# Performance work log

Measured on AMD Instinct MI355X. Metric: run time of the kernel, lower is better.

## Reference

```python
import jax, jax.numpy as jnp
import numpy as np

B, N, D = 4, 512, 128
TAU = 0.5
EPS = 1e-9

def setup_inputs() -> dict:
    key = jax.random.key(0)
    ks = jax.random.split(key, 6)
    sc = 0.05  # weight scale for numerical sanity
    return {
        "entity_states": jax.random.normal(ks[0], (B, N, D), dtype=jnp.float32),
        "Wp": jax.random.normal(ks[1], (D, D), dtype=jnp.float32) * sc,
        "bp": jnp.zeros((D,), dtype=jnp.float32),
        "edge_logits": jax.random.normal(ks[2], (N, N), dtype=jnp.float32),
        "W1": jax.random.normal(ks[3], (2 * D, D), dtype=jnp.float32) * sc,
        "b1": jnp.zeros((D,), dtype=jnp.float32),
        "W2": jax.random.normal(ks[4], (D, D), dtype=jnp.float32) * sc,
        "b2": jnp.zeros((D,), dtype=jnp.float32),
        "u_noise": jax.random.uniform(ks[5], (N, N), dtype=jnp.float32),
    }

def reference(entity_states, Wp, bp, edge_logits, W1, b1, W2, b2, u_noise):
    b, n, d = entity_states.shape
    # entity projection
    proj = entity_states @ Wp + bp  # (B,N,D)
    # gumbel-softmax adjacency (row-wise softmax over sources)
    g = -jnp.log(-jnp.log(u_noise + EPS) + EPS)
    A = jax.nn.softmax((edge_logits + g) / TAU, axis=-1)  # (N,N)
    # split concat-MLP first layer: combined = [source_j, target_i]
    W1_src, W1_tgt = W1[:d], W1[d:]
    s = proj @ W1_src  # (B,N,D) contribution of source j
    t = proj @ W1_tgt  # (B,N,D) contribution of target i
    # h[b,i,j,:] = relu(s[b,j] + t[b,i] + b1)
    h = jax.nn.relu(s[:, None, :, :] + t[:, :, None, :] + b1)  # (B,N,N,D)
    msg = h @ W2 + b2  # (B,N,N,D)
    # weighted aggregation over sources j with A[i,j]
    upd = jnp.einsum('ij,bijd->bid', A, msg)  # (B,N,D)
    next_state = entity_states + upd
    return next_state, jnp.broadcast_to(A, (b, n, n))
```

## Files before the change

kernel.cpp:

```cpp
#include <hip/hip_runtime.h>
#include <math.h>

#define Bv 4
#define Nv 512
#define Dv 128
#define BND (Bv*Nv*Dv)
#define NN  (Nv*Nv)
#define EPSv 1e-9f

typedef float f4 __attribute__((ext_vector_type(4)));

__device__ __forceinline__ f4 relu4(f4 z) {
#if __has_builtin(__builtin_elementwise_max)
    return __builtin_elementwise_max(z, (f4)0.0f);
#else
    z.x = fmaxf(z.x, 0.0f); z.y = fmaxf(z.y, 0.0f);
    z.z = fmaxf(z.z, 0.0f); z.w = fmaxf(z.w, 0.0f);
    return z;
#endif
}

__global__ __launch_bounds__(256) void k_prep(
    const float* __restrict__ ES, const float* __restrict__ Wp,
    const float* __restrict__ bp, const float* __restrict__ W1,
    const float* __restrict__ b1, const float* __restrict__ EL,
    const float* __restrict__ UN,
    float* __restrict__ s_out, float* __restrict__ t_out,
    float* __restrict__ A_out)
{
    __shared__ float es[4][Dv];
    __shared__ float pr[4][Dv];
    __shared__ float sred[4];
    const int bi = blockIdx.x;
    const int t  = threadIdx.x;

    {
        const int row = bi;
        const float u0 = UN[row*Nv + t];
        const float u1 = UN[row*Nv + t + 256];
        const float g0 = -logf(-logf(u0 + EPSv) + EPSv);
        const float g1 = -logf(-logf(u1 + EPSv) + EPSv);
        const float z0 = (EL[row*Nv + t]       + g0) * 2.0f;
        const float z1 = (EL[row*Nv + t + 256] + g1) * 2.0f;

        float m = fmaxf(z0, z1);
        #pragma unroll
        for (int off = 32; off >= 1; off >>= 1)
            m = fmaxf(m, __shfl_xor(m, off, 64));
        if ((t & 63) == 0) sred[t >> 6] = m;
        __syncthreads();
        m = fmaxf(fmaxf(sred[0], sred[1]), fmaxf(sred[2], sred[3]));

        const float e0 = expf(z0 - m);
        const float e1 = expf(z1 - m);
        float ssum = e0 + e1;
        #pragma unroll
        for (int off = 32; off >= 1; off >>= 1)
            ssum += __shfl_xor(ssum, off, 64);
        __syncthreads();
        if ((t & 63) == 0) sred[t >> 6] = ssum;
        __syncthreads();
        const float inv = 1.0f / (sred[0] + sred[1] + sred[2] + sred[3]);
        const float a0 = e0 * inv;
        const float a1 = e1 * inv;
        #pragma unroll
        for (int bb = 0; bb < Bv; ++bb) {
            A_out[bb*NN + row*Nv + t]       = a0;
            A_out[bb*NN + row*Nv + t + 256] = a1;
        }
    }

    const int row0 = bi * 4;
    const int c  = t & 127;
    const int rg = t >> 7;

    for (int idx = t; idx < 4*Dv; idx += 256)
        es[idx >> 7][idx & 127] = ES[(row0 + (idx >> 7))*Dv + (idx & 127)];
    __syncthreads();

    {
        float acc[2];
        const float bpc = bp[c];
        acc[0] = bpc; acc[1] = bpc;
        #pragma unroll 8
        for (int k = 0; k < Dv; ++k) {
            const float w = Wp[k*Dv + c];
            acc[0] = fmaf(es[rg*2][k],   w, acc[0]);
            acc[1] = fmaf(es[rg*2+1][k], w, acc[1]);
        }
        pr[rg*2][c]   = acc[0];
        pr[rg*2+1][c] = acc[1];
    }
    __syncthreads();

    float sacc0 = b1[c], sacc1 = sacc0, tacc0 = 0.0f, tacc1 = 0.0f;
    #pragma unroll 8
    for (int k = 0; k < Dv; ++k) {
        const float ws_ = W1[k*Dv + c];
        const float wt_ = W1[(Dv + k)*Dv + c];
        const float p0 = pr[rg*2][k];
        const float p1 = pr[rg*2+1][k];
        sacc0 = fmaf(p0, ws_, sacc0);
        sacc1 = fmaf(p1, ws_, sacc1);
        tacc0 = fmaf(p0, wt_, tacc0);
        tacc1 = fmaf(p1, wt_, tacc1);
    }
    const int ra = (row0 + rg*2)*Dv + c;
    s_out[ra]      = sacc0;
    s_out[ra + Dv] = sacc1;
    t_out[ra]      = tacc0;
    t_out[ra + Dv] = tacc1;
}

__global__ __launch_bounds__(256) void k_main(
    const float* __restrict__ s_buf, const float* __restrict__ t_buf,
    const float* __restrict__ A0,    const float* __restrict__ ES,
    const float* __restrict__ W2,    const float* __restrict__ b2,
    float* __restrict__ out)
{
    __shared__ float A_lds[8][Nv];
    __shared__ f4    part[8][8][32];
    __shared__ float hsum[8][Dv];
    const int i0 = blockIdx.x * 8;
    const int b  = blockIdx.y;
    const int t  = threadIdx.x;
    const int dq = t & 31;
    const int jg = t >> 5;

    {
        const f4* __restrict__ src = (const f4*)(A0 + i0*Nv);
        f4* dst = (f4*)(&A_lds[0][0]);
        #pragma unroll
        for (int u = 0; u < 4; ++u)
            dst[t + u*256] = src[t + u*256];
    }

    f4 tv[8];
    #pragma unroll
    for (int r = 0; r < 8; ++r)
        tv[r] = *(const f4*)(t_buf + (b*Nv + i0 + r)*Dv + dq*4);

    f4 acc[8];
    #pragma unroll
    for (int r = 0; r < 8; ++r) acc[r] = (f4)0.0f;

    __syncthreads();

    const float* __restrict__ sb = s_buf + (size_t)b*Nv*Dv + dq*4;
    const int j0 = jg*64;
    for (int j4 = j0; j4 < j0 + 64; j4 += 4) {
        f4 a[8];
        #pragma unroll
        for (int r = 0; r < 8; ++r)
            a[r] = *(const f4*)(&A_lds[r][j4]);
        #pragma unroll
        for (int u = 0; u < 4; ++u) {
            const f4 sv = *(const f4*)(sb + (j4 + u)*Dv);
            #pragma unroll
            for (int r = 0; r < 8; ++r) {
                f4 z = relu4(sv + tv[r]);
                acc[r] += a[r][u] * z;
            }
        }
    }

    #pragma unroll
    for (int r = 0; r < 8; ++r) part[jg][r][dq] = acc[r];
    __syncthreads();
    {
        const int ri = t >> 5;
        f4 s = part[0][ri][dq];
        #pragma unroll
        for (int g = 1; g < 8; ++g) s += part[g][ri][dq];
        *(f4*)(&hsum[ri][dq*4]) = s;
    }
    __syncthreads();

    const int cg = t & 63;
    const int rg = t >> 6;
    const int c0 = 2*cg;
    const int r0 = 2*rg;
    float o00 = b2[c0], o01 = b2[c0+1];
    float o10 = o00,    o11 = o01;
    for (int k4 = 0; k4 < Dv; k4 += 4) {
        const f4 h0 = *(const f4*)(&hsum[r0][k4]);
        const f4 h1 = *(const f4*)(&hsum[r0+1][k4]);
        #pragma unroll
        for (int u = 0; u < 4; ++u) {
            const float2 w = *(const float2*)(W2 + (k4 + u)*Dv + c0);
            o00 = fmaf(h0[u], w.x, o00);
            o01 = fmaf(h0[u], w.y, o01);
            o10 = fmaf(h1[u], w.x, o10);
            o11 = fmaf(h1[u], w.y, o11);
        }
    }
    const int ro0 = (b*Nv + i0 + r0)*Dv + c0;
    const int ro1 = ro0 + Dv;
    const float2 e0 = *(const float2*)(ES + ro0);
    const float2 e1 = *(const float2*)(ES + ro1);
    float2 v0, v1;
    v0.x = e0.x + o00; v0.y = e0.y + o01;
    v1.x = e1.x + o10; v1.y = e1.y + o11;
    *(float2*)(out + ro0) = v0;
    *(float2*)(out + ro1) = v1;
}

extern "C" void kernel_launch(void* const* d_in, const int* in_sizes, int n_in,
                              void* d_out, int out_size, void* d_ws, size_t ws_size,
                              hipStream_t stream) {
    (void)in_sizes; (void)n_in; (void)out_size; (void)ws_size;
    const float* ES = (const float*)d_in[0];
    const float* Wp = (const float*)d_in[1];
    const float* bp = (const float*)d_in[2];
    const float* EL = (const float*)d_in[3];
    const float* W1 = (const float*)d_in[4];
    const float* b1 = (const float*)d_in[5];
    const float* W2 = (const float*)d_in[6];
    const float* b2 = (const float*)d_in[7];
    const float* UN = (const float*)d_in[8];

    float* out   = (float*)d_out;
    float* A_out = out + BND;

    float* s_buf = (float*)d_ws;
    float* t_buf = s_buf + BND;

    k_prep<<<512, 256, 0, stream>>>(ES, Wp, bp, W1, b1, EL, UN,
                                    s_buf, t_buf, A_out);
    k_main<<<dim3(Nv/8, Bv), 256, 0, stream>>>(s_buf, t_buf, A_out, ES, W2, b2,
                                               out);
}
```

Measured before the change: 109.2 us.

## Double k_main threads, prefetch source rows, use fast exp/log in prep

k_main now runs 512 threads per block, so each thread handles 32 source rows instead of 64. The s_buf loads are software-prefetched one step ahead, and the partial-sum reduction and W2 epilogue are reorganised for the larger block. The prep kernel switches to the fast __logf/__expf intrinsics for the Gumbel-softmax. The aim is more waves in flight to hide memory latency and a shorter serial loop, at the cost of a larger LDS reduction buffer, higher register pressure from the prefetch, and slightly lower accuracy in the softmax.

```diff
diff --git a/kernel.cpp b/kernel.cpp
--- a/kernel.cpp
+++ b/kernel.cpp
@@ -38,8 +38,8 @@
         const int row = bi;
         const float u0 = UN[row*Nv + t];
         const float u1 = UN[row*Nv + t + 256];
-        const float g0 = -logf(-logf(u0 + EPSv) + EPSv);
-        const float g1 = -logf(-logf(u1 + EPSv) + EPSv);
+        const float g0 = -__logf(-__logf(u0 + EPSv) + EPSv);
+        const float g1 = -__logf(-__logf(u1 + EPSv) + EPSv);
         const float z0 = (EL[row*Nv + t]       + g0) * 2.0f;
         const float z1 = (EL[row*Nv + t + 256] + g1) * 2.0f;
 
@@ -51,8 +51,8 @@
         __syncthreads();
         m = fmaxf(fmaxf(sred[0], sred[1]), fmaxf(sred[2], sred[3]));
 
-        const float e0 = expf(z0 - m);
-        const float e1 = expf(z1 - m);
+        const float e0 = __expf(z0 - m);
+        const float e1 = __expf(z1 - m);
         float ssum = e0 + e1;
         #pragma unroll
         for (int off = 32; off >= 1; off >>= 1)
@@ -112,14 +112,14 @@
     t_out[ra + Dv] = tacc1;
 }
 
-__global__ __launch_bounds__(256) void k_main(
+__global__ __launch_bounds__(512, 2) void k_main(
     const float* __restrict__ s_buf, const float* __restrict__ t_buf,
     const float* __restrict__ A0,    const float* __restrict__ ES,
     const float* __restrict__ W2,    const float* __restrict__ b2,
     float* __restrict__ out)
 {
     __shared__ float A_lds[8][Nv];
-    __shared__ f4    part[8][8][32];
+    __shared__ f4    part[16][8][32];
     __shared__ float hsum[8][Dv];
     const int i0 = blockIdx.x * 8;
     const int b  = blockIdx.y;
@@ -130,9 +130,8 @@
     {
         const f4* __restrict__ src = (const f4*)(A0 + i0*Nv);
         f4* dst = (f4*)(&A_lds[0][0]);
-        #pragma unroll
-        for (int u = 0; u < 4; ++u)
-            dst[t + u*256] = src[t + u*256];
+        dst[t]       = src[t];
+        dst[t + 512] = src[t + 512];
     }
 
     f4 tv[8];
@@ -147,62 +146,66 @@
     __syncthreads();
 
     const float* __restrict__ sb = s_buf + (size_t)b*Nv*Dv + dq*4;
-    const int j0 = jg*64;
-    for (int j4 = j0; j4 < j0 + 64; j4 += 4) {
+    const int j0 = jg * 32;
+
+    f4 svn0 = *(const f4*)(sb + (j0+0)*Dv);
+    f4 svn1 = *(const f4*)(sb + (j0+1)*Dv);
+    f4 svn2 = *(const f4*)(sb + (j0+2)*Dv);
+    f4 svn3 = *(const f4*)(sb + (j0+3)*Dv);
+
+    #pragma unroll
+    for (int jj = 0; jj < 32; jj += 4) {
+        const int j4 = j0 + jj;
+        const f4 sv0 = svn0, sv1 = svn1, sv2 = svn2, sv3 = svn3;
+        if (jj < 28) {
+            svn0 = *(const f4*)(sb + (j4+4)*Dv);
+            svn1 = *(const f4*)(sb + (j4+5)*Dv);
+            svn2 = *(const f4*)(sb + (j4+6)*Dv);
+            svn3 = *(const f4*)(sb + (j4+7)*Dv);
+        }
         f4 a[8];
         #pragma unroll
         for (int r = 0; r < 8; ++r)
             a[r] = *(const f4*)(&A_lds[r][j4]);
         #pragma unroll
-        for (int u = 0; u < 4; ++u) {
-            const f4 sv = *(const f4*)(sb + (j4 + u)*Dv);
-            #pragma unroll
-            for (int r = 0; r < 8; ++r) {
-                f4 z = relu4(sv + tv[r]);
-                acc[r] += a[r][u] * z;
-            }
+        for (int r = 0; r < 8; ++r) {
+            acc[r] += a[r][0] * relu4(sv0 + tv[r]);
+            acc[r] += a[r][1] * relu4(sv1 + tv[r]);
+            acc[r] += a[r][2] * relu4(sv2 + tv[r]);
+            acc[r] += a[r][3] * relu4(sv3 + tv[r]);
         }
     }
 
     #pragma unroll
     for (int r = 0; r < 8; ++r) part[jg][r][dq] = acc[r];
     __syncthreads();
-    {
+    if (t < 256) {
         const int ri = t >> 5;
         f4 s = part[0][ri][dq];
         #pragma unroll
-        for (int g = 1; g < 8; ++g) s += part[g][ri][dq];
+        for (int g = 1; g < 16; ++g) s += part[g][ri][dq];
         *(f4*)(&hsum[ri][dq*4]) = s;
     }
     __syncthreads();
 
     const int cg = t & 63;
-    const int rg = t >> 6;
+    const int rr = t >> 6;
     const int c0 = 2*cg;
-    const int r0 = 2*rg;
-    float o00 = b2[c0], o01 = b2[c0+1];
-    float o10 = o00,    o11 = o01;
+    float o0 = b2[c0], o1 = b2[c0+1];
+    #pragma unroll 8
     for (int k4 = 0; k4 < Dv; k4 += 4) {
-        const f4 h0 = *(const f4*)(&hsum[r0][k4]);
-        const f4 h1 = *(const f4*)(&hsum[r0+1][k4]);
+        const f4 h = *(const f4*)(&hsum[rr][k4]);
         #pragma unroll
         for (int u = 0; u < 4; ++u) {
             const float2 w = *(const float2*)(W2 + (k4 + u)*Dv + c0);
-            o00 = fmaf(h0[u], w.x, o00);
-            o01 = fmaf(h0[u], w.y, o01);
-            o10 = fmaf(h1[u], w.x, o10);
-            o11 = fmaf(h1[u], w.y, o11);
-        }
-    }
-    const int ro0 = (b*Nv + i0 + r0)*Dv + c0;
-    const int ro1 = ro0 + Dv;
-    const float2 e0 = *(const float2*)(ES + ro0);
-    const float2 e1 = *(const float2*)(ES + ro1);
-    float2 v0, v1;
-    v0.x = e0.x + o00; v0.y = e0.y + o01;
-    v1.x = e1.x + o10; v1.y = e1.y + o11;
-    *(float2*)(out + ro0) = v0;
-    *(float2*)(out + ro1) = v1;
+            o0 = fmaf(h[u], w.x, o0);
+            o1 = fmaf(h[u], w.y, o1);
+        }
+    }
+    const int ro = (b*Nv + i0 + rr)*Dv + c0;
+    const float2 e = *(const float2*)(ES + ro);
+    float2 v; v.x = e.x + o0; v.y = e.y + o1;
+    *(float2*)(out + ro) = v;
 }
 
 extern "C" void kernel_launch(void* const* d_in, const int* in_sizes, int n_in,
@@ -227,6 +230,6 @@
 
     k_prep<<<512, 256, 0, stream>>>(ES, Wp, bp, W1, b1, EL, UN,
                                     s_buf, t_buf, A_out);
-    k_main<<<dim3(Nv/8, Bv), 256, 0, stream>>>(s_buf, t_buf, A_out, ES, W2, b2,
+    k_main<<<dim3(Nv/8, Bv), 512, 0, stream>>>(s_buf, t_buf, A_out, ES, W2, b2,
                                                out);
 }
```

Result: faster. 102.5 us (-6.1%).
